# Optimization experiments

Measured on AMD Instinct MI355X. Metric: run time of the kernel, lower is better.

The kernel has to match this reference:

```python
import jax, jax.numpy as jnp
import numpy as np

N, E, L = 2048, 16384, 8
IN_DIM, HID, PE, EDGE_DIM, OUT_DIM, HEADS, MASK_DIM = 9, 256, 20, 2, 6, 8, 6
ENC = HID - PE
HD = HID // HEADS

def _bn(x, g, b):
    # BatchNorm1d in training-mode math (batch statistics, biased var), dropout disabled
    mu = x.mean(0)
    var = ((x - mu) ** 2).mean(0)
    return (x - mu) * jax.lax.rsqrt(var + 1e-5) * g + b

def _leaky(x):
    return jnp.where(x > 0, x, 0.01 * x)

def setup_inputs():
    key = jax.random.key(0)
    ks = iter(jax.random.split(key, 64))
    def p(*shape):
        return jax.random.normal(next(ks), shape, jnp.float32) * 0.05
    return dict(
        x=jax.random.normal(next(ks), (N, IN_DIM), jnp.float32),
        pe=jax.random.normal(next(ks), (N, PE), jnp.float32),
        edge_attr=jax.random.normal(next(ks), (E, EDGE_DIM), jnp.float32),
        mask_value=jax.random.normal(next(ks), (MASK_DIM,), jnp.float32),
        enc_w=p(IN_DIM, ENC), enc_b=p(ENC),
        in_g=jnp.ones((ENC,)), in_b=jnp.zeros((ENC,)),
        pe_g=jnp.ones((PE,)), pe_b=jnp.zeros((PE,)),
        gine_ew=p(L, EDGE_DIM, HID), gine_eb=p(L, HID),
        gine_mw=p(L, HID, HID), gine_mb=p(L, HID),
        attn_inw=p(L, HID, 3 * HID), attn_inb=p(L, 3 * HID),
        attn_outw=p(L, HID, HID), attn_outb=p(L, HID),
        mlp1w=p(L, HID, 2 * HID), mlp1b=p(L, 2 * HID),
        mlp2w=p(L, 2 * HID, HID), mlp2b=p(L, HID),
        n1g=jnp.ones((L, HID)), n1b=jnp.zeros((L, HID)),
        n2g=jnp.ones((L, HID)), n2b=jnp.zeros((L, HID)),
        n3g=jnp.ones((L, HID)), n3b=jnp.zeros((L, HID)),
        obn_g=jnp.ones((L, HID)), obn_b=jnp.zeros((L, HID)),
        pd_g=jnp.ones((HID,)), pd_b=jnp.zeros((HID,)),
        dec1w=p(HID, HID), dec1b=p(HID),
        dec2w=p(HID, OUT_DIM), dec2b=p(OUT_DIM),
        edge_index=jax.random.randint(next(ks), (2, E), 0, N, jnp.int32),
        mask=jax.random.randint(next(ks), (N, MASK_DIM), 0, 2, jnp.int32).astype(bool),
    )

def reference(x, pe, edge_attr, mask_value, enc_w, enc_b, in_g, in_b, pe_g, pe_b,
              gine_ew, gine_eb, gine_mw, gine_mb, attn_inw, attn_inb, attn_outw, attn_outb,
              mlp1w, mlp1b, mlp2w, mlp2b, n1g, n1b, n2g, n2b, n3g, n3b, obn_g, obn_b,
              pd_g, pd_b, dec1w, dec1b, dec2w, dec2b, edge_index, mask):
    src, dst = edge_index[0], edge_index[1]
    # masked-feature replacement on x[:, 3:3+mask_dim]
    blk = jnp.where(mask, mask_value[None, :], x[:, 3:3 + MASK_DIM])
    x = x.at[:, 3:3 + MASK_DIM].set(blk)
    h = _bn(_leaky(x @ enc_w + enc_b), in_g, in_b)
    h = jnp.concatenate([h, _bn(pe, pe_g, pe_b)], axis=1)  # [N, HID]
    for l in range(L):
        xin = h
        # GINEConv (eps=0): nn((1+eps)*x_i + sum_j relu(x_j + lin(e_ji)))
        eemb = edge_attr @ gine_ew[l] + gine_eb[l]            # [E, HID]
        msg = jax.nn.relu(xin[src] + eemb)                    # gather + fuse
        agg = jax.ops.segment_sum(msg, dst, num_segments=N)   # scatter-add
        hl = _leaky((xin + agg) @ gine_mw[l] + gine_mb[l])
        hl = _bn(hl + xin, n1g[l], n1b[l])                    # local branch + residual + norm1
        # global multi-head self-attention (single graph -> dense batch, no padding)
        qkv = xin @ attn_inw[l] + attn_inb[l]
        q, k, v = [t.reshape(N, HEADS, HD) for t in jnp.split(qkv, 3, axis=1)]
        a = jax.nn.softmax(jnp.einsum('nhd,mhd->hnm', q, k) / np.float32(np.sqrt(HD)), axis=-1)
        o = jnp.einsum('hnm,mhd->nhd', a, v).reshape(N, HID)
        ha = _bn(o @ attn_outw[l] + attn_outb[l] + xin, n2g[l], n2b[l])  # attn branch + residual + norm2
        out = hl + ha
        out = out + (jax.nn.relu(out @ mlp1w[l] + mlp1b[l]) @ mlp2w[l] + mlp2b[l])  # GPS FFN
        out = _bn(out, n3g[l], n3b[l])
        h = _bn(out, obn_g[l], obn_b[l])                      # outer per-layer BatchNorm
    h = _bn(h, pd_g, pd_b)
    return _leaky(h @ dec1w + dec1b) @ dec2w + dec2b
```

## Files before the change

kernel.cpp:

```cpp
#include <hip/hip_runtime.h>
#include <hip/hip_bf16.h>

typedef __hip_bfloat16 bf16;
typedef __attribute__((ext_vector_type(8))) short v8s;
typedef __attribute__((ext_vector_type(4))) float v4f;

#define NN 2048
#define EE 16384
#define LLAYERS 8
#define HIDD 256
#define ENCD 236
#define PED 20
#define BN_EPS 1e-5f
#define ATT_SCALE 0.17677669529663687f
#define KSPLIT 4

__device__ __forceinline__ float b2f(bf16 v){ return __bfloat162float(v); }
__device__ __forceinline__ float bs2f(unsigned short u){ return __uint_as_float(((unsigned)u) << 16); }
__device__ __forceinline__ unsigned short f2bs(float f){
  bf16 h = __float2bfloat16(f);
  union { bf16 b; unsigned short u; } cv; cv.b = h; return cv.u;
}
__device__ __forceinline__ float ld1f(const void* p, size_t i, int f){
  return f ? b2f(((const bf16*)p)[i]) : ((const float*)p)[i];
}

__global__ void k_detect2(const unsigned int* __restrict__ xw,
                          const unsigned char* __restrict__ mk, int* __restrict__ flags){
  __shared__ int sh[256];
  int t = threadIdx.x;
  if (blockIdx.x == 0){
    int cnt = 0;
    for (int i = t; i < 8192; i += 256){
      unsigned b = (xw[i] >> 8) & 0xffu;
      unsigned v = b & 0x7fu;
      if (v == 0u || (v >= 0x30u && v <= 0x43u)) cnt++;
    }
    sh[t] = cnt; __syncthreads();
    for (int s = 128; s; s >>= 1){ if (t < s) sh[t] += sh[t+s]; __syncthreads(); }
    if (t == 0) flags[0] = (sh[0] > 6000) ? 1 : 0;
  } else {
    int acc = 0;
    for (int i = t; i < NN*6; i += 256){
      unsigned b = mk[i]; int m = i & 3;
      if ((m == 1 && b == 0x3Fu) || (m == 0 && b == 0x80u)) acc |= 4;
      if (b == 0x3Fu || b == 0x80u) acc |= 2;
      if (m != 0 && b != 0u) acc |= 1;
    }
    sh[t] = acc; __syncthreads();
    for (int s = 128; s; s >>= 1){ if (t < s) sh[t] |= sh[t+s]; __syncthreads(); }
    if (t == 0){
      int a = sh[0];
      flags[1] = (a & 4) ? 2 : (a & 2) ? 3 : (a & 1) ? 1 : 0;
    }
  }
}

__global__ void k_tw(const void* __restrict__ src, unsigned short* __restrict__ dst,
                     int K, int N, const int* __restrict__ dflag){
  __shared__ float tile[32][33];
  int n0 = blockIdx.x*32, k0 = blockIdx.y*32, b = blockIdx.z;
  int t = threadIdx.x, x = t & 31, y = t >> 5;
  int f = dflag[0];
  size_t so = (size_t)b*K*N, dofs = (size_t)b*N*K;
  #pragma unroll
  for (int i = 0; i < 4; i++){
    int k = k0 + y + 8*i;
    tile[y+8*i][x] = ld1f(src, so + (size_t)k*N + n0 + x, f);
  }
  __syncthreads();
  #pragma unroll
  for (int i = 0; i < 4; i++){
    int n = n0 + y + 8*i;
    dst[dofs + (size_t)n*K + k0 + x] = f2bs(tile[x][y+8*i]);
  }
}
__global__ void k_tw3(const void* __restrict__ sA, const void* __restrict__ sB,
                      const void* __restrict__ sC, unsigned short* __restrict__ dst,
                      const int* __restrict__ dflag){
  __shared__ float tile[32][33];
  int z = blockIdx.z;
  const void* src = (z < 8) ? sA : (z < 16) ? sB : sC;
  int b = (z < 8) ? z : (z < 16) ? z - 8 : 0;
  int n0 = blockIdx.x*32, k0 = blockIdx.y*32;
  int t = threadIdx.x, x = t & 31, y = t >> 5;
  int f = dflag[0];
  size_t so = (size_t)b*65536, dofs = (size_t)z*65536;
  #pragma unroll
  for (int i = 0; i < 4; i++){
    int k = k0 + y + 8*i;
    tile[y+8*i][x] = ld1f(src, so + (size_t)k*256 + n0 + x, f);
  }
  __syncthreads();
  #pragma unroll
  for (int i = 0; i < 4; i++){
    int n = n0 + y + 8*i;
    dst[dofs + (size_t)n*256 + k0 + x] = f2bs(tile[x][y+8*i]);
  }
}

__global__ void k_csr_count(const int* __restrict__ ei, int* __restrict__ counts){
  int e = blockIdx.x*256 + threadIdx.x;
  if (e < EE) atomicAdd(&counts[ei[EE + e]], 1);
}
__global__ void k_csr_scan(const int* __restrict__ counts, int* __restrict__ rowstart,
                           int* __restrict__ cursor){
  __shared__ int ts[256];
  int t = threadIdx.x, base = t*8;
  int loc[8]; int s = 0;
  #pragma unroll
  for (int i = 0; i < 8; i++){ loc[i] = s; s += counts[base + i]; }
  ts[t] = s; __syncthreads();
  for (int off = 1; off < 256; off <<= 1){
    int v = (t >= off) ? ts[t - off] : 0;
    __syncthreads();
    ts[t] += v;
    __syncthreads();
  }
  int excl = ts[t] - s;
  #pragma unroll
  for (int i = 0; i < 8; i++){
    int v = excl + loc[i];
    rowstart[base + i] = v; cursor[base + i] = v;
  }
  if (t == 255) rowstart[2048] = ts[255];
}
__global__ void k_csr_fill(const int* __restrict__ ei, const void* __restrict__ ea,
                           const int* __restrict__ dflag, int* __restrict__ cursor,
                           int* __restrict__ csr_src, float2* __restrict__ csr_a){
  int e = blockIdx.x*256 + threadIdx.x;
  if (e >= EE) return;
  int s = ei[e], d = ei[EE + e];
  int pos = atomicAdd(&cursor[d], 1);
  int f = dflag[0];
  csr_src[pos] = s;
  csr_a[pos] = make_float2(ld1f(ea, (size_t)e*2, f), ld1f(ea, (size_t)e*2 + 1, f));
}

__global__ void k_encode(const void* __restrict__ x, const void* __restrict__ mval,
                         const void* __restrict__ mask, const int* __restrict__ flags,
                         const void* __restrict__ w, const void* __restrict__ b,
                         float* __restrict__ out){
  __shared__ float xr[16];
  int r = blockIdx.x, t = threadIdx.x;
  int f = flags[0];
  if (t < 9){
    float v = ld1f(x, (size_t)r*9 + t, f);
    if (t >= 3){
      int j = t - 3;
      size_t idx = (size_t)r*6 + j;
      int mf = flags[1];
      bool mm;
      if      (mf == 0) mm = ((const int*)mask)[idx] != 0;
      else if (mf == 1) mm = ((const unsigned char*)mask)[idx] != 0;
      else if (mf == 2) mm = ((const unsigned short*)mask)[idx] != 0;
      else              mm = ((const unsigned int*)mask)[idx] != 0;
      if (mm) v = ld1f(mval, j, f);
    }
    xr[t] = v;
  }
  __syncthreads();
  if (t < ENCD){
    float acc = ld1f(b, t, f);
    #pragma unroll
    for (int k = 0; k < 9; k++) acc = fmaf(xr[k], ld1f(w, (size_t)k*ENCD + t, f), acc);
    out[r*ENCD + t] = acc > 0.f ? acc : 0.01f*acc;
  }
}
__global__ void k_cvt(const void* __restrict__ src, const int* __restrict__ dflag,
                      float* __restrict__ dst, int n){
  int i = blockIdx.x*256 + threadIdx.x;
  if (i < n) dst[i] = ld1f(src, i, dflag[0]);
}
__global__ void k_bn2x(const float* __restrict__ encb, const float* __restrict__ pef,
                       const void* __restrict__ eg, const void* __restrict__ eb,
                       const void* __restrict__ pg, const void* __restrict__ pb,
                       const int* __restrict__ dflag,
                       float* __restrict__ scE, float* __restrict__ shE,
                       float* __restrict__ scP, float* __restrict__ shP){
  int cb = blockIdx.x, t = threadIdx.x;
  const float* src; int ld, c; const void *g, *b; float *sc, *sh;
  if (cb < ENCD){ src = encb; ld = ENCD; c = cb; g = eg; b = eb; sc = scE; sh = shE; }
  else          { src = pef;  ld = PED;  c = cb - ENCD; g = pg; b = pb; sc = scP; sh = shP; }
  float s = 0.f, q = 0.f;
  for (int r = t; r < NN; r += 256){ float v = src[(size_t)r*ld + c]; s += v; q += v*v; }
  __shared__ float ss[256], qs[256];
  ss[t] = s; qs[t] = q; __syncthreads();
  for (int k = 128; k; k >>= 1){ if (t < k){ ss[t] += ss[t+k]; qs[t] += qs[t+k]; } __syncthreads(); }
  if (t == 0){
    int f = dflag[0];
    float mu  = ss[0] * (1.f/NN);
    float var = qs[0] * (1.f/NN) - mu*mu;
    float r1  = rsqrtf(var + BN_EPS);
    float scv = ld1f(g, c, f) * r1;
    sc[c] = scv; sh[c] = ld1f(b, c, f) - mu*scv;
  }
}
__global__ void k_concat(unsigned short* __restrict__ h, const float* __restrict__ encb,
                         const float* __restrict__ pef,
                         const float* __restrict__ scE, const float* __restrict__ shE,
                         const float* __restrict__ scP, const float* __restrict__ shP){
  int i = blockIdx.x*256 + threadIdx.x;
  int r = i >> 8, c = i & 255;
  float v;
  if (c < ENCD) v = encb[r*ENCD + c]*scE[c] + shE[c];
  else { int j = c - ENCD; v = pef[r*PED + j]*scP[j] + shP[j]; }
  h[i] = f2bs(v);
}

__device__ __forceinline__ void dualbn(const float* slab, int c, int f,
                                       const void* g1, size_t g1o,
                                       const void* g2, size_t g2o,
                                       const void* b2, size_t b2o,
                                       float& sc, float& sh){
  float mu  = slab[2*c] * (1.f/NN);
  float var = slab[2*c+1] * (1.f/NN) - mu*mu;
  float r1  = rsqrtf(var + BN_EPS);
  float gg  = ld1f(g1, g1o + c, f);
  float zv  = var * r1 * r1 * gg * gg;
  float r2  = rsqrtf(zv + BN_EPS);
  sc = r1 * gg * r2 * ld1f(g2, g2o + c, f);
  sh = ld1f(b2, b2o + c, f) - mu*sc;
}
__device__ __forceinline__ void singlebn(const float* slab, int c, int f,
                                         const void* g, size_t go,
                                         const void* b, size_t bo,
                                         float& sc, float& sh){
  float mu  = slab[2*c] * (1.f/NN);
  float var = slab[2*c+1] * (1.f/NN) - mu*mu;
  float r1  = rsqrtf(var + BN_EPS);
  sc = ld1f(g, go + c, f) * r1;
  sh = ld1f(b, bo + c, f) - mu*sc;
}

__device__ void dev_gather(const unsigned short* __restrict__ h0,
                           const float* __restrict__ t3, int hsrc,
                           const float* __restrict__ slabH,
                           const void* Hg1, size_t Hg1o, const void* Hg2, size_t Hg2o,
                           const void* Hb2, size_t Hb2o,
                           int dst, const int* __restrict__ rowstart,
                           const int* __restrict__ csr_src, const float2* __restrict__ csr_a,
                           const void* __restrict__ w, size_t woff,
                           const void* __restrict__ b, size_t boff, int f,
                           float* __restrict__ agg){
  int c = threadIdx.x;
  float sc = 1.f, sh = 0.f;
  if (hsrc) dualbn(slabH, c, f, Hg1, Hg1o, Hg2, Hg2o, Hb2, Hb2o, sc, sh);
  float w0 = ld1f(w, woff + c, f), w1 = ld1f(w, woff + HIDD + c, f);
  float bb = ld1f(b, boff + c, f);
  int beg = rowstart[dst], end = rowstart[dst + 1];
  float acc = 0.f;
  for (int i = beg; i < end; i++){
    int s = csr_src[i]; float2 a = csr_a[i];
    float hv = hsrc ? t3[(size_t)s*HIDD + c]*sc + sh : bs2f(h0[(size_t)s*HIDD + c]);
    float m = hv + a.x*w0 + a.y*w1 + bb;
    acc += fmaxf(m, 0.f);
  }
  agg[(size_t)dst*HIDD + c] = acc;
}

template<int ACT, int APATH, int RESMODE, int OUTBF, int STATS>
__device__ void dev_mgemm(char* sm, int bn, int bm,
    const unsigned short* __restrict__ Ab, const float* __restrict__ Af, int hsrc,
    const float* __restrict__ agg,
    const float* __restrict__ Opart, const float* __restrict__ lsum,
    const float* __restrict__ t1p, const float* __restrict__ t2p,
    const float* __restrict__ slabH,
    const void* Hg1, size_t Hg1o, const void* Hg2, size_t Hg2o,
    const void* Hb2, size_t Hb2o,
    const void* Pg, size_t Pgo, const void* Pb, size_t Pbo,
    const float* __restrict__ slab1,
    const void* g1, size_t g1o, const void* b1, size_t b1o,
    const float* __restrict__ slab2,
    const void* g2, size_t g2o, const void* b2, size_t b2o,
    const unsigned short* __restrict__ Wt,
    const void* __restrict__ bias, size_t boff,
    void* __restrict__ C, int N_, int K, int qcols, float qscale,
    float* __restrict__ stats, int f){
  unsigned short (*As)[40] = (unsigned short(*)[40])sm;
  unsigned short (*Bs)[40] = (unsigned short(*)[40])(sm + 5120);
  constexpr bool NEEDH = (APATH <= 1 || RESMODE == 1 || APATH == 4);
  constexpr size_t TB = 10240 + (NEEDH ? 2048 : 0);
  float* scH = (float*)(sm + 10240); float* shH = scH + 256;
  float* tc1 = (float*)(sm + TB);    float* th1 = tc1 + 256;
  float* tc2 = th1 + 256;            float* th2 = tc2 + 256;
  int tid = threadIdx.x, L = tid & 63, wv = tid >> 6;
  int wm = wv >> 1, wn = wv & 1;
  int quad = L >> 4, lo = L & 15;
  int srow = tid >> 2, sk = (tid & 3)*8;

  if (NEEDH && (hsrc || APATH == 4)){
    int c = tid;
    float s, h;
    dualbn(slabH, c, f, Hg1, Hg1o, Hg2, Hg2o, Hb2, Hb2o, s, h);
    if (APATH == 4){
      float mu  = slabH[2*c] * (1.f/NN);
      float var = slabH[2*c+1] * (1.f/NN) - mu*mu;
      float muh = mu*s + h, varh = var*s*s;
      float rp  = rsqrtf(varh + BN_EPS);
      float sp  = ld1f(Pg, Pgo + c, f) * rp;
      float hp  = ld1f(Pb, Pbo + c, f) - muh*sp;
      s = s*sp; h = h*sp + hp;
    }
    scH[c] = s; shH[c] = h;
  }
  if (APATH == 3 || RESMODE == 2){
    int c = tid;
    float s, h;
    singlebn(slab1, c, f, g1, g1o, b1, b1o, s, h); tc1[c] = s; th1[c] = h;
    singlebn(slab2, c, f, g2, g2o, b2, b2o, s, h); tc2[c] = s; th2[c] = h;
  }
  __syncthreads();

  v4f acc[2][2];
  #pragma unroll
  for (int i = 0; i < 2; i++)
    #pragma unroll
    for (int j = 0; j < 2; j++) acc[i][j] = (v4f){0.f,0.f,0.f,0.f};

  for (int kk = 0; kk < K; kk += 32){
    int row = bm + srow, c0 = kk + sk;
    uint4 aval;
    if (APATH == 0 || APATH == 4){
      if (APATH == 0 && !hsrc){
        aval = *(const uint4*)(Ab + (size_t)row*K + c0);
      } else {
        unsigned short us8[8];
        #pragma unroll
        for (int j = 0; j < 8; j++){
          int c = c0 + j;
          us8[j] = f2bs(Af[(size_t)row*K + c]*scH[c] + shH[c]);
        }
        aval = *(const uint4*)us8;
      }
    } else if (APATH == 1){
      unsigned short us8[8];
      if (!hsrc){
        uint4 araw = *(const uint4*)(Ab + (size_t)row*K + c0);
        unsigned parts[4] = {araw.x, araw.y, araw.z, araw.w};
        #pragma unroll
        for (int p = 0; p < 4; p++){
          us8[2*p]   = f2bs(bs2f((unsigned short)(parts[p] & 0xffffu)) + agg[(size_t)row*K + c0 + 2*p]);
          us8[2*p+1] = f2bs(bs2f((unsigned short)(parts[p] >> 16))     + agg[(size_t)row*K + c0 + 2*p + 1]);
        }
      } else {
        #pragma unroll
        for (int j = 0; j < 8; j++){
          int c = c0 + j;
          us8[j] = f2bs(Af[(size_t)row*K + c]*scH[c] + shH[c] + agg[(size_t)row*K + c]);
        }
      }
      aval = *(const uint4*)us8;
    } else if (APATH == 2){
      int hd = c0 >> 5, d0 = c0 & 31;
      size_t mlb = ((size_t)row*8 + hd)*KSPLIT;
      float inv = 1.f / (lsum[mlb] + lsum[mlb+1] + lsum[mlb+2] + lsum[mlb+3]);
      const float* Op = Opart + mlb*32 + d0;
      unsigned short us8[8];
      #pragma unroll
      for (int j = 0; j < 8; j++){
        float v = (Op[j] + Op[32+j] + Op[64+j] + Op[96+j])*inv;
        us8[j] = f2bs(v);
      }
      aval = *(const uint4*)us8;
    } else {
      unsigned short us8[8];
      #pragma unroll
      for (int j = 0; j < 8; j++){
        int c = c0 + j;
        float v = t1p[(size_t)row*HIDD + c]*tc1[c] + th1[c]
                + t2p[(size_t)row*HIDD + c]*tc2[c] + th2[c];
        us8[j] = f2bs(v);
      }
      aval = *(const uint4*)us8;
    }
    uint4 bval = *(const uint4*)(Wt + (size_t)(bn + srow)*K + c0);
    __syncthreads();
    *(uint4*)&As[srow][sk] = aval;
    *(uint4*)&Bs[srow][sk] = bval;
    __syncthreads();
    v8s af[2], bfr[2];
    af[0]  = *(const v8s*)&As[wm*32 + lo][quad*8];
    af[1]  = *(const v8s*)&As[wm*32 + 16 + lo][quad*8];
    bfr[0] = *(const v8s*)&Bs[wn*32 + lo][quad*8];
    bfr[1] = *(const v8s*)&Bs[wn*32 + 16 + lo][quad*8];
    #pragma unroll
    for (int mi = 0; mi < 2; mi++)
      #pragma unroll
      for (int nj = 0; nj < 2; nj++)
        acc[mi][nj] = __builtin_amdgcn_mfma_f32_16x16x32_bf16(af[mi], bfr[nj], acc[mi][nj], 0, 0, 0);
  }

  float ssum[2] = {0.f, 0.f}, ssq[2] = {0.f, 0.f};
  #pragma unroll
  for (int mi = 0; mi < 2; mi++){
    #pragma unroll
    for (int nj = 0; nj < 2; nj++){
      int col = bn + wn*32 + nj*16 + lo;
      float bv = ld1f(bias, boff + col, f);
      #pragma unroll
      for (int r = 0; r < 4; r++){
        int row = bm + wm*32 + mi*16 + quad*4 + r;
        float t = acc[mi][nj][r] + bv;
        if (ACT == 1) t = fmaxf(t, 0.f);
        if (ACT == 2) t = t > 0.f ? t : 0.01f*t;
        if (qcols && col < qcols) t *= qscale;
        if (RESMODE == 1)
          t += hsrc ? (Af[(size_t)row*N_ + col]*scH[col] + shH[col])
                    : bs2f(Ab[(size_t)row*N_ + col]);
        if (RESMODE == 2)
          t += t1p[(size_t)row*HIDD + col]*tc1[col] + th1[col]
             + t2p[(size_t)row*HIDD + col]*tc2[col] + th2[col];
        if (STATS){ ssum[nj] += t; ssq[nj] += t*t; }
        if (OUTBF) ((unsigned short*)C)[(size_t)row*N_ + col] = f2bs(t);
        else       ((float*)C)[(size_t)row*N_ + col] = t;
      }
    }
  }
  if (STATS){
    #pragma unroll
    for (int nj = 0; nj < 2; nj++){
      float s = ssum[nj], q = ssq[nj];
      s += __shfl_xor(s, 16, 64); s += __shfl_xor(s, 32, 64);
      q += __shfl_xor(q, 16, 64); q += __shfl_xor(q, 32, 64);
      if (quad == 0){
        int col = bn + wn*32 + nj*16 + lo;
        atomicAdd(&stats[2*col],   s);
        atomicAdd(&stats[2*col+1], q);
      }
    }
  }
}

__device__ void dev_attn(char* sm, const unsigned short* __restrict__ qkv,
                         int q0, int hd, int ks,
                         float* __restrict__ Opart, float* __restrict__ lsum){
  unsigned short (*Ks)[40] = (unsigned short(*)[40])sm;
  unsigned short (*Vt)[66] = (unsigned short(*)[66])(sm + 5120);
  unsigned short (*Ps)[16][68] = (unsigned short(*)[16][68])(sm + 9344);
  int tid = threadIdx.x, L = tid & 63, wv = tid >> 6;
  int quad = L >> 4, lo = L & 15;
  int skey = tid >> 2, sd = (tid & 3)*8;

  v8s qf = *(const v8s*)(qkv + (size_t)(q0 + 16*wv + lo)*768 + hd*32 + quad*8);
  v4f o0 = (v4f){0.f,0.f,0.f,0.f}, o1 = (v4f){0.f,0.f,0.f,0.f};
  float lrow[4] = {0.f, 0.f, 0.f, 0.f};

  int kbeg = ks * (NN/KSPLIT), kend = kbeg + NN/KSPLIT;
  for (int kt = kbeg; kt < kend; kt += 64){
    const unsigned short* kp = qkv + (size_t)(kt + skey)*768 + 256 + hd*32 + sd;
    uint4 kraw = *(const uint4*)kp;
    uint4 vraw = *(const uint4*)(kp + 256);
    __syncthreads();
    *(uint4*)&Ks[skey][sd] = kraw;
    {
      unsigned short vs[8]; *(uint4*)vs = vraw;
      #pragma unroll
      for (int j = 0; j < 8; j++) Vt[sd + j][skey] = vs[j];
    }
    __syncthreads();
    v4f s[4];
    #pragma unroll
    for (int sub = 0; sub < 4; sub++){
      v8s kf = *(const v8s*)&Ks[sub*16 + lo][quad*8];
      s[sub] = __builtin_amdgcn_mfma_f32_16x16x32_bf16(qf, kf, (v4f){0.f,0.f,0.f,0.f}, 0, 0, 0);
    }
    #pragma unroll
    for (int r = 0; r < 4; r++){
      #pragma unroll
      for (int sub = 0; sub < 4; sub++){
        float p = __expf(s[sub][r]);
        Ps[wv][quad*4 + r][sub*16 + lo] = f2bs(p);
        lrow[r] += p;
      }
    }
    #pragma unroll
    for (int kc = 0; kc < 2; kc++){
      v8s pf  = *(const v8s*)&Ps[wv][lo][kc*32 + quad*8];
      v8s v0f = *(const v8s*)&Vt[lo][kc*32 + quad*8];
      v8s v1f = *(const v8s*)&Vt[16 + lo][kc*32 + quad*8];
      o0 = __builtin_amdgcn_mfma_f32_16x16x32_bf16(pf, v0f, o0, 0, 0, 0);
      o1 = __builtin_amdgcn_mfma_f32_16x16x32_bf16(pf, v1f, o1, 0, 0, 0);
    }
  }
  #pragma unroll
  for (int r = 0; r < 4; r++){
    float v = lrow[r];
    #pragma unroll
    for (int off = 1; off < 16; off <<= 1) v += __shfl_xor(v, off, 64);
    lrow[r] = v;
  }
  #pragma unroll
  for (int r = 0; r < 4; r++){
    int row = q0 + 16*wv + quad*4 + r;
    size_t base = (((size_t)row*8 + hd)*KSPLIT + ks)*32;
    Opart[base + lo]      = o0[r];
    Opart[base + 16 + lo] = o1[r];
    if (lo == 0) lsum[((size_t)row*8 + hd)*KSPLIT + ks] = lrow[r];
  }
}

__launch_bounds__(256)
__global__ void k_d1(const unsigned short* __restrict__ h0, const float* __restrict__ t3,
                     int hsrc, const float* __restrict__ slabH,
                     const void* Hg1, size_t Hg1o, const void* Hg2, size_t Hg2o,
                     const void* Hb2, size_t Hb2o,
                     const unsigned short* __restrict__ qkw,
                     const void* qb, size_t qbo, unsigned short* __restrict__ qkvb,
                     const int* __restrict__ rowstart, const int* __restrict__ csr_src,
                     const float2* __restrict__ csr_a,
                     const void* gw, size_t gwo, const void* gb, size_t gbo,
                     float* __restrict__ agg, const int* __restrict__ dflagp){
  __shared__ char sm[12288];
  int f = dflagp[0];
  int bx = blockIdx.x;
  if (bx < 384){
    dev_mgemm<0,0,0,1,0>(sm, (bx % 12)*64, (bx / 12)*64, h0, t3, hsrc,
        nullptr, nullptr, nullptr, nullptr, nullptr,
        slabH, Hg1, Hg1o, Hg2, Hg2o, Hb2, Hb2o, nullptr, 0, nullptr, 0,
        nullptr, nullptr, 0, nullptr, 0, nullptr, nullptr, 0, nullptr, 0,
        qkw, qb, qbo, qkvb, 768, 256, 256, ATT_SCALE, nullptr, f);
  } else {
    dev_gather(h0, t3, hsrc, slabH, Hg1, Hg1o, Hg2, Hg2o, Hb2, Hb2o,
               bx - 384, rowstart, csr_src, csr_a, gw, gwo, gb, gbo, f, agg);
  }
}

__launch_bounds__(256)
__global__ void k_d2(const unsigned short* __restrict__ h0, const float* __restrict__ t3,
                     int hsrc, const float* __restrict__ slabH,
                     const void* Hg1, size_t Hg1o, const void* Hg2, size_t Hg2o,
                     const void* Hb2, size_t Hb2o,
                     const float* __restrict__ agg,
                     const unsigned short* __restrict__ gmw,
                     const void* gmb, size_t gmbo,
                     float* __restrict__ t1, float* __restrict__ stats1,
                     const unsigned short* __restrict__ qkvb,
                     float* __restrict__ Opart, float* __restrict__ lsum,
                     const int* __restrict__ dflagp){
  __shared__ char sm[18432];
  int bx = blockIdx.x;
  if (bx < 128){
    int f = dflagp[0];
    dev_mgemm<2,1,1,0,1>(sm, (bx & 3)*64, (bx >> 2)*64, h0, t3, hsrc,
        agg, nullptr, nullptr, nullptr, nullptr,
        slabH, Hg1, Hg1o, Hg2, Hg2o, Hb2, Hb2o, nullptr, 0, nullptr, 0,
        nullptr, nullptr, 0, nullptr, 0, nullptr, nullptr, 0, nullptr, 0,
        gmw, gmb, gmbo, t1, 256, 256, 0, 1.f, stats1, f);
  } else {
    int b = bx - 128;
    dev_attn(sm, qkvb, (b & 31)*64, (b >> 5) & 7, b >> 8, Opart, lsum);
  }
}

__launch_bounds__(256)
__global__ void k_g3(const unsigned short* __restrict__ h0, const float* __restrict__ t3,
                     int hsrc, const float* __restrict__ slabH,
                     const void* Hg1, size_t Hg1o, const void* Hg2, size_t Hg2o,
                     const void* Hb2, size_t Hb2o,
                     const float* __restrict__ Opart, const float* __restrict__ lsum,
                     const unsigned short* __restrict__ aow,
                     const void* aob, size_t aobo,
                     float* __restrict__ t2, float* __restrict__ stats2,
                     const int* __restrict__ dflagp){
  __shared__ char sm[12288];
  dev_mgemm<0,2,1,0,1>(sm, blockIdx.x*64, blockIdx.y*64, h0, t3, hsrc,
      nullptr, Opart, lsum, nullptr, nullptr,
      slabH, Hg1, Hg1o, Hg2, Hg2o, Hb2, Hb2o, nullptr, 0, nullptr, 0,
      nullptr, nullptr, 0, nullptr, 0, nullptr, nullptr, 0, nullptr, 0,
      aow, aob, aobo, t2, 256, 256, 0, 1.f, stats2, dflagp[0]);
}

__launch_bounds__(256)
__global__ void k_g4(const float* __restrict__ t1, const float* __restrict__ t2,
                     const float* __restrict__ slab1,
                     const void* g1, size_t g1o, const void* b1, size_t b1o,
                     const float* __restrict__ slab2,
                     const void* g2, size_t g2o, const void* b2, size_t b2o,
                     const unsigned short* __restrict__ m1w,
                     const void* m1b, size_t m1bo,
                     unsigned short* __restrict__ u, const int* __restrict__ dflagp){
  __shared__ char sm[14336];
  dev_mgemm<1,3,0,1,0>(sm, blockIdx.x*64, blockIdx.y*64, nullptr, nullptr, 0,
      nullptr, nullptr, nullptr, t1, t2,
      nullptr, nullptr, 0, nullptr, 0, nullptr, 0, nullptr, 0, nullptr, 0,
      slab1, g1, g1o, b1, b1o, slab2, g2, g2o, b2, b2o,
      m1w, m1b, m1bo, u, 512, 256, 0, 1.f, nullptr, dflagp[0]);
}

__launch_bounds__(256)
__global__ void k_g5(const unsigned short* __restrict__ u,
                     const float* __restrict__ t1, const float* __restrict__ t2,
                     const float* __restrict__ slab1,
                     const void* g1, size_t g1o, const void* b1, size_t b1o,
                     const float* __restrict__ slab2,
                     const void* g2, size_t g2o, const void* b2, size_t b2o,
                     const unsigned short* __restrict__ m2w,
                     const void* m2b, size_t m2bo,
                     float* __restrict__ t3, float* __restrict__ stats3,
                     const int* __restrict__ dflagp){
  __shared__ char sm[14336];
  dev_mgemm<0,0,2,0,1>(sm, blockIdx.x*64, blockIdx.y*64, u, nullptr, 0,
      nullptr, nullptr, nullptr, t1, t2,
      nullptr, nullptr, 0, nullptr, 0, nullptr, 0, nullptr, 0, nullptr, 0,
      slab1, g1, g1o, b1, b1o, slab2, g2, g2o, b2, b2o,
      m2w, m2b, m2bo, t3, 256, 512, 0, 1.f, stats3, dflagp[0]);
}

__launch_bounds__(256)
__global__ void k_gdec(const float* __restrict__ t3, const float* __restrict__ slabH,
                       const void* Hg1, size_t Hg1o, const void* Hg2, size_t Hg2o,
                       const void* Hb2, size_t Hb2o,
                       const void* Pg, const void* Pb,
                       const unsigned short* __restrict__ d1w,
                       const void* d1bv, unsigned short* __restrict__ d1b,
                       const int* __restrict__ dflagp){
  __shared__ char sm[12288];
  dev_mgemm<2,4,0,1,0>(sm, blockIdx.x*64, blockIdx.y*64, nullptr, t3, 1,
      nullptr, nullptr, nullptr, nullptr, nullptr,
      slabH, Hg1, Hg1o, Hg2, Hg2o, Hb2, Hb2o, Pg, 0, Pb, 0,
      nullptr, nullptr, 0, nullptr, 0, nullptr, nullptr, 0, nullptr, 0,
      d1w, d1bv, 0, d1b, 256, 256, 0, 1.f, nullptr, dflagp[0]);
}

__global__ void k_dec2(const unsigned short* __restrict__ d1, const void* __restrict__ w,
                       const void* __restrict__ b, const int* __restrict__ dflag,
                       void* __restrict__ out){
  int r = blockIdx.x, t = threadIdx.x;
  int f = dflag[0];
  float a = bs2f(d1[(size_t)r*HIDD + t]);
  float p[6];
  #pragma unroll
  for (int n = 0; n < 6; n++) p[n] = a * ld1f(w, (size_t)t*6 + n, f);
  #pragma unroll
  for (int off = 32; off >= 1; off >>= 1)
    #pragma unroll
    for (int n = 0; n < 6; n++) p[n] += __shfl_down(p[n], off, 64);
  __shared__ float red[4][6];
  int wvv = t >> 6, ln = t & 63;
  if (ln == 0)
    #pragma unroll
    for (int n = 0; n < 6; n++) red[wvv][n] = p[n];
  __syncthreads();
  if (t < 6){
    float s = red[0][t] + red[1][t] + red[2][t] + red[3][t] + ld1f(b, t, f);
    if (f) ((bf16*)out)[r*6 + t] = __float2bfloat16(s);
    else   ((float*)out)[r*6 + t] = s;
  }
}

extern "C" void kernel_launch(void* const* d_in, const int* in_sizes, int n_in,
                              void* d_out, int out_size, void* d_ws, size_t ws_size,
                              hipStream_t stream){
  const void* x          = d_in[0];
  const void* pe         = d_in[1];
  const void* edge_attr  = d_in[2];
  const void* mask_value = d_in[3];
  const void* enc_w = d_in[4];  const void* enc_b = d_in[5];
  const void* in_g  = d_in[6];  const void* in_b  = d_in[7];
  const void* pe_g  = d_in[8];  const void* pe_b  = d_in[9];
  const void* gine_ew = d_in[10]; const void* gine_eb = d_in[11];
  const void* gine_mw = d_in[12]; const void* gine_mb = d_in[13];
  const void* attn_inw  = d_in[14]; const void* attn_inb  = d_in[15];
  const void* attn_outw = d_in[16]; const void* attn_outb = d_in[17];
  const void* mlp1w = d_in[18]; const void* mlp1b = d_in[19];
  const void* mlp2w = d_in[20]; const void* mlp2b = d_in[21];
  const void* n1g = d_in[22]; const void* n1b = d_in[23];
  const void* n2g = d_in[24]; const void* n2b = d_in[25];
  const void* n3g = d_in[26]; const void* n3b = d_in[27];
  const void* obn_g = d_in[28]; const void* obn_b = d_in[29];
  const void* pd_g  = d_in[30]; const void* pd_b  = d_in[31];
  const void* dec1w = d_in[32]; const void* dec1b = d_in[33];
  const void* dec2w = d_in[34]; const void* dec2b = d_in[35];
  const int*  edge_index = (const int*)d_in[36];
  const void* mask = d_in[37];
  (void)in_sizes; (void)n_in; (void)out_size; (void)ws_size;

  char* cur = (char*)d_ws;
  auto alloc = [&](size_t bytes)->char*{
    char* p = cur; cur += (bytes + 63) & ~(size_t)63; return p;
  };
  int*   flags = (int*)alloc(64);
  int*   dflag = flags;
  float* scE = (float*)alloc(ENCD*4); float* shE = (float*)alloc(ENCD*4);
  float* scP = (float*)alloc(PED*4);  float* shP = (float*)alloc(PED*4);
  int*   counts = (int*)alloc(2048*4);
  float* stats1 = (float*)alloc((size_t)LLAYERS*512*4);
  float* stats2 = (float*)alloc((size_t)LLAYERS*512*4);
  float* stats3 = (float*)alloc((size_t)LLAYERS*512*4);
  size_t zero_bytes = 2048*4 + 3*(size_t)LLAYERS*512*4;
  int*    rowstart = (int*)alloc(2052*4);
  int*    cursor   = (int*)alloc(2048*4);
  int*    csr_src  = (int*)alloc((size_t)EE*4);
  float2* csr_a    = (float2*)alloc((size_t)EE*8);
  unsigned short* h    = (unsigned short*)alloc((size_t)NN*HIDD*2);
  float*          t1   = (float*)alloc((size_t)NN*HIDD*4);
  float*          agg  = (float*)alloc((size_t)NN*HIDD*4);
  float*          t3   = (float*)alloc((size_t)NN*HIDD*4);
  unsigned short* qkvb = (unsigned short*)alloc((size_t)NN*768*2);
  float*          Opart= (float*)alloc((size_t)NN*8*KSPLIT*32*4);
  float*          lsum = (float*)alloc((size_t)NN*8*KSPLIT*4);
  unsigned short* sqw  = (unsigned short*)alloc((size_t)17*65536*2);
  unsigned short* ainw_t = (unsigned short*)alloc((size_t)8*768*256*2);
  unsigned short* m1w_t  = (unsigned short*)alloc((size_t)8*512*256*2);
  unsigned short* m2w_t  = (unsigned short*)alloc((size_t)8*256*512*2);
  unsigned short* gmw_t   = sqw;
  unsigned short* aoutw_t = sqw + (size_t)8*65536;
  unsigned short* d1w_t   = sqw + (size_t)16*65536;
  float* t2 = agg;
  unsigned short* u    = qkvb;
  float*          encb = (float*)qkvb;
  float*          pef  = (float*)qkvb + (size_t)NN*ENCD;
  unsigned short* d1b  = (unsigned short*)Opart;

  k_detect2<<<2, 256, 0, stream>>>((const unsigned int*)x, (const unsigned char*)mask, flags);
  hipMemsetAsync(counts, 0, zero_bytes, stream);
  k_csr_count<<<EE/256, 256, 0, stream>>>(edge_index, counts);
  k_csr_scan<<<1, 256, 0, stream>>>(counts, rowstart, cursor);
  k_csr_fill<<<EE/256, 256, 0, stream>>>(edge_index, edge_attr, dflag, cursor, csr_src, csr_a);
  k_tw3<<<dim3(8, 8, 17), 256, 0, stream>>>(gine_mw, attn_outw, dec1w, sqw, dflag);
  k_tw<<<dim3(24, 8, 8), 256, 0, stream>>>(attn_inw, ainw_t, 256, 768, dflag);
  k_tw<<<dim3(16, 8, 8), 256, 0, stream>>>(mlp1w,    m1w_t,  256, 512, dflag);
  k_tw<<<dim3(8, 16, 8), 256, 0, stream>>>(mlp2w,    m2w_t,  512, 256, dflag);
  k_encode<<<NN, 256, 0, stream>>>(x, mask_value, mask, flags, enc_w, enc_b, encb);
  k_cvt<<<(NN*PED + 255)/256, 256, 0, stream>>>(pe, dflag, pef, NN*PED);
  k_bn2x<<<256, 256, 0, stream>>>(encb, pef, in_g, in_b, pe_g, pe_b, dflag, scE, shE, scP, shP);
  k_concat<<<NN*HIDD/256, 256, 0, stream>>>(h, encb, pef, scE, shE, scP, shP);

  for (int l = 0; l < LLAYERS; l++){
    int hs = (l > 0);
    const float* slH = stats3 + (size_t)(hs ? (l-1) : 0)*512;
    size_t o3 = (size_t)(hs ? (l-1) : 0)*256;
    k_d1<<<2432, 256, 0, stream>>>(h, t3, hs, slH, n3g, o3, obn_g, o3, obn_b, o3,
        ainw_t + (size_t)l*196608, attn_inb, (size_t)l*768, qkvb,
        rowstart, csr_src, csr_a,
        gine_ew, (size_t)l*2*HIDD, gine_eb, (size_t)l*HIDD, agg, dflag);
    k_d2<<<1152, 256, 0, stream>>>(h, t3, hs, slH, n3g, o3, obn_g, o3, obn_b, o3,
        agg, gmw_t + (size_t)l*65536, gine_mb, (size_t)l*256, t1, stats1 + (size_t)l*512,
        qkvb, Opart, lsum, dflag);
    k_g3<<<dim3(4,32), 256, 0, stream>>>(h, t3, hs, slH, n3g, o3, obn_g, o3, obn_b, o3,
        Opart, lsum, aoutw_t + (size_t)l*65536, attn_outb, (size_t)l*256,
        t2, stats2 + (size_t)l*512, dflag);
    k_g4<<<dim3(8,32), 256, 0, stream>>>(t1, t2,
        stats1 + (size_t)l*512, n1g, (size_t)l*256, n1b, (size_t)l*256,
        stats2 + (size_t)l*512, n2g, (size_t)l*256, n2b, (size_t)l*256,
        m1w_t + (size_t)l*131072, mlp1b, (size_t)l*512, u, dflag);
    k_g5<<<dim3(4,32), 256, 0, stream>>>(u, t1, t2,
        stats1 + (size_t)l*512, n1g, (size_t)l*256, n1b, (size_t)l*256,
        stats2 + (size_t)l*512, n2g, (size_t)l*256, n2b, (size_t)l*256,
        m2w_t + (size_t)l*131072, mlp2b, (size_t)l*256, t3, stats3 + (size_t)l*512, dflag);
  }

  k_gdec<<<dim3(4,32), 256, 0, stream>>>(t3, stats3 + (size_t)7*512,
      n3g, (size_t)7*256, obn_g, (size_t)7*256, obn_b, (size_t)7*256,
      pd_g, pd_b, d1w_t, dec1b, d1b, dflag);
  k_dec2<<<NN, 256, 0, stream>>>(d1b, dec2w, dec2b, dflag, d_out);
}
```

Before: 937.9 us.

## Split attention into standalone 512-thread kernel and co-launch GINE GEMM with out-proj

Attention now runs in its own kernel with 512-thread blocks covering 128 queries, using half-width K/V staging loads so each block shares a larger K/V tile across more waves. The GINE message GEMM moves out of the attention launch and is co-scheduled with the attention out-projection GEMM in one launch. The pe conversion is folded into the encoder kernel, which drops one launch. The aim is better K/V reuse and better load balance between the heterogeneous block types, at the cost of narrower global loads and different occupancy.

Result: faster. 788.1 us (-16.0%).

```diff
diff --git a/kernel.cpp b/kernel.cpp
--- a/kernel.cpp
+++ b/kernel.cpp
@@ -140,7 +140,8 @@
 __global__ void k_encode(const void* __restrict__ x, const void* __restrict__ mval,
                          const void* __restrict__ mask, const int* __restrict__ flags,
                          const void* __restrict__ w, const void* __restrict__ b,
-                         float* __restrict__ out){
+                         const void* __restrict__ pe,
+                         float* __restrict__ out, float* __restrict__ pef){
   __shared__ float xr[16];
   int r = blockIdx.x, t = threadIdx.x;
   int f = flags[0];
@@ -165,12 +166,10 @@
     #pragma unroll
     for (int k = 0; k < 9; k++) acc = fmaf(xr[k], ld1f(w, (size_t)k*ENCD + t, f), acc);
     out[r*ENCD + t] = acc > 0.f ? acc : 0.01f*acc;
-  }
-}
-__global__ void k_cvt(const void* __restrict__ src, const int* __restrict__ dflag,
-                      float* __restrict__ dst, int n){
-  int i = blockIdx.x*256 + threadIdx.x;
-  if (i < n) dst[i] = ld1f(src, i, dflag[0]);
+  } else {
+    int j = t - ENCD;
+    pef[(size_t)r*PED + j] = ld1f(pe, (size_t)r*PED + j, f);
+  }
 }
 __global__ void k_bn2x(const float* __restrict__ encb, const float* __restrict__ pef,
                        const void* __restrict__ eg, const void* __restrict__ eb,
@@ -432,15 +431,18 @@
   }
 }
 
-__device__ void dev_attn(char* sm, const unsigned short* __restrict__ qkv,
-                         int q0, int hd, int ks,
-                         float* __restrict__ Opart, float* __restrict__ lsum){
-  unsigned short (*Ks)[40] = (unsigned short(*)[40])sm;
-  unsigned short (*Vt)[66] = (unsigned short(*)[66])(sm + 5120);
-  unsigned short (*Ps)[16][68] = (unsigned short(*)[16][68])(sm + 9344);
+__launch_bounds__(512)
+__global__ void k_d2(const unsigned short* __restrict__ qkv,
+                     float* __restrict__ Opart, float* __restrict__ lsum){
+  __shared__ unsigned short Ks[64][40];
+  __shared__ unsigned short Vt[32][66];
+  __shared__ unsigned short Ps[8][16][68];
+  int b = blockIdx.x;
+  int qt = b & 15, hd = (b >> 4) & 7, ks = b >> 7;
+  int q0 = qt*128;
   int tid = threadIdx.x, L = tid & 63, wv = tid >> 6;
   int quad = L >> 4, lo = L & 15;
-  int skey = tid >> 2, sd = (tid & 3)*8;
+  int skey = tid >> 3, sd = (tid & 7)*4;
 
   v8s qf = *(const v8s*)(qkv + (size_t)(q0 + 16*wv + lo)*768 + hd*32 + quad*8);
   v4f o0 = (v4f){0.f,0.f,0.f,0.f}, o1 = (v4f){0.f,0.f,0.f,0.f};
@@ -449,14 +451,14 @@
   int kbeg = ks * (NN/KSPLIT), kend = kbeg + NN/KSPLIT;
   for (int kt = kbeg; kt < kend; kt += 64){
     const unsigned short* kp = qkv + (size_t)(kt + skey)*768 + 256 + hd*32 + sd;
-    uint4 kraw = *(const uint4*)kp;
-    uint4 vraw = *(const uint4*)(kp + 256);
+    uint2 kraw = *(const uint2*)kp;
+    uint2 vraw = *(const uint2*)(kp + 256);
     __syncthreads();
-    *(uint4*)&Ks[skey][sd] = kraw;
+    *(uint2*)&Ks[skey][sd] = kraw;
     {
-      unsigned short vs[8]; *(uint4*)vs = vraw;
+      unsigned short vs[4]; *(uint2*)vs = vraw;
       #pragma unroll
-      for (int j = 0; j < 8; j++) Vt[sd + j][skey] = vs[j];
+      for (int j = 0; j < 4; j++) Vt[sd + j][skey] = vs[j];
     }
     __syncthreads();
     v4f s[4];
@@ -527,7 +529,7 @@
 }
 
 __launch_bounds__(256)
-__global__ void k_d2(const unsigned short* __restrict__ h0, const float* __restrict__ t3,
+__global__ void k_g3(const unsigned short* __restrict__ h0, const float* __restrict__ t3,
                      int hsrc, const float* __restrict__ slabH,
                      const void* Hg1, size_t Hg1o, const void* Hg2, size_t Hg2o,
                      const void* Hb2, size_t Hb2o,
@@ -535,40 +537,28 @@
                      const unsigned short* __restrict__ gmw,
                      const void* gmb, size_t gmbo,
                      float* __restrict__ t1, float* __restrict__ stats1,
-                     const unsigned short* __restrict__ qkvb,
-                     float* __restrict__ Opart, float* __restrict__ lsum,
+                     const float* __restrict__ Opart, const float* __restrict__ lsum,
+                     const unsigned short* __restrict__ aow,
+                     const void* aob, size_t aobo,
+                     float* __restrict__ t2, float* __restrict__ stats2,
                      const int* __restrict__ dflagp){
-  __shared__ char sm[18432];
+  __shared__ char sm[12288];
+  int f = dflagp[0];
   int bx = blockIdx.x;
   if (bx < 128){
-    int f = dflagp[0];
     dev_mgemm<2,1,1,0,1>(sm, (bx & 3)*64, (bx >> 2)*64, h0, t3, hsrc,
         agg, nullptr, nullptr, nullptr, nullptr,
         slabH, Hg1, Hg1o, Hg2, Hg2o, Hb2, Hb2o, nullptr, 0, nullptr, 0,
         nullptr, nullptr, 0, nullptr, 0, nullptr, nullptr, 0, nullptr, 0,
         gmw, gmb, gmbo, t1, 256, 256, 0, 1.f, stats1, f);
   } else {
-    int b = bx - 128;
-    dev_attn(sm, qkvb, (b & 31)*64, (b >> 5) & 7, b >> 8, Opart, lsum);
-  }
-}
-
-__launch_bounds__(256)
-__global__ void k_g3(const unsigned short* __restrict__ h0, const float* __restrict__ t3,
-                     int hsrc, const float* __restrict__ slabH,
-                     const void* Hg1, size_t Hg1o, const void* Hg2, size_t Hg2o,
-                     const void* Hb2, size_t Hb2o,
-                     const float* __restrict__ Opart, const float* __restrict__ lsum,
-                     const unsigned short* __restrict__ aow,
-                     const void* aob, size_t aobo,
-                     float* __restrict__ t2, float* __restrict__ stats2,
-                     const int* __restrict__ dflagp){
-  __shared__ char sm[12288];
-  dev_mgemm<0,2,1,0,1>(sm, blockIdx.x*64, blockIdx.y*64, h0, t3, hsrc,
-      nullptr, Opart, lsum, nullptr, nullptr,
-      slabH, Hg1, Hg1o, Hg2, Hg2o, Hb2, Hb2o, nullptr, 0, nullptr, 0,
-      nullptr, nullptr, 0, nullptr, 0, nullptr, nullptr, 0, nullptr, 0,
-      aow, aob, aobo, t2, 256, 256, 0, 1.f, stats2, dflagp[0]);
+    int bb = bx - 128;
+    dev_mgemm<0,2,1,0,1>(sm, (bb & 3)*64, (bb >> 2)*64, h0, t3, hsrc,
+        nullptr, Opart, lsum, nullptr, nullptr,
+        slabH, Hg1, Hg1o, Hg2, Hg2o, Hb2, Hb2o, nullptr, 0, nullptr, 0,
+        nullptr, nullptr, 0, nullptr, 0, nullptr, nullptr, 0, nullptr, 0,
+        aow, aob, aobo, t2, 256, 256, 0, 1.f, stats2, f);
+  }
 }
 
 __launch_bounds__(256)
@@ -722,8 +712,7 @@
   k_tw<<<dim3(24, 8, 8), 256, 0, stream>>>(attn_inw, ainw_t, 256, 768, dflag);
   k_tw<<<dim3(16, 8, 8), 256, 0, stream>>>(mlp1w,    m1w_t,  256, 512, dflag);
   k_tw<<<dim3(8, 16, 8), 256, 0, stream>>>(mlp2w,    m2w_t,  512, 256, dflag);
-  k_encode<<<NN, 256, 0, stream>>>(x, mask_value, mask, flags, enc_w, enc_b, encb);
-  k_cvt<<<(NN*PED + 255)/256, 256, 0, stream>>>(pe, dflag, pef, NN*PED);
+  k_encode<<<NN, 256, 0, stream>>>(x, mask_value, mask, flags, enc_w, enc_b, pe, encb, pef);
   k_bn2x<<<256, 256, 0, stream>>>(encb, pef, in_g, in_b, pe_g, pe_b, dflag, scE, shE, scP, shP);
   k_concat<<<NN*HIDD/256, 256, 0, stream>>>(h, encb, pef, scE, shE, scP, shP);
 
@@ -735,10 +724,9 @@
         ainw_t + (size_t)l*196608, attn_inb, (size_t)l*768, qkvb,
         rowstart, csr_src, csr_a,
         gine_ew, (size_t)l*2*HIDD, gine_eb, (size_t)l*HIDD, agg, dflag);
-    k_d2<<<1152, 256, 0, stream>>>(h, t3, hs, slH, n3g, o3, obn_g, o3, obn_b, o3,
+    k_d2<<<512, 512, 0, stream>>>(qkvb, Opart, lsum);
+    k_g3<<<256, 256, 0, stream>>>(h, t3, hs, slH, n3g, o3, obn_g, o3, obn_b, o3,
         agg, gmw_t + (size_t)l*65536, gine_mb, (size_t)l*256, t1, stats1 + (size_t)l*512,
-        qkvb, Opart, lsum, dflag);
-    k_g3<<<dim3(4,32), 256, 0, stream>>>(h, t3, hs, slH, n3g, o3, obn_g, o3, obn_b, o3,
         Opart, lsum, aoutw_t + (size_t)l*65536, attn_outb, (size_t)l*256,
         t2, stats2 + (size_t)l*512, dflag);
     k_g4<<<dim3(8,32), 256, 0, stream>>>(t1, t2,
```
